# Optimization experiments

Hardware: AMD Instinct MI355X
Metric: run time of the kernel (lower is better)

Reference implementation:

```python
import jax, jax.numpy as jnp
from jax import lax
import numpy as np

B, C, H, W = 8, 256, 64, 64
DSTATE, DCONV, EXPAND = 16, 4, 2
DI = EXPAND * C          # 512 d_inner
DTR = (C + 15) // 16     # 16 dt_rank = ceil(d_model/16)

# ---------- helpers ----------

def _ln(x, g, b):
    m = x.mean(-1, keepdims=True)
    v = x.var(-1, keepdims=True)
    return (x - m) * lax.rsqrt(v + 1e-5) * g + b


def _bn(x, g, b):  # BatchNorm2d, training-mode batch stats
    m = x.mean((0, 2, 3), keepdims=True)
    v = x.var((0, 2, 3), keepdims=True)
    return (x - m) * lax.rsqrt(v + 1e-5) * g[None, :, None, None] + b[None, :, None, None]


def _gn(x, g, b, groups=32):
    Bb, Cc, Hh, Ww = x.shape
    xr = x.reshape(Bb, groups, Cc // groups, Hh, Ww)
    m = xr.mean((2, 3, 4), keepdims=True)
    v = xr.var((2, 3, 4), keepdims=True)
    xr = (xr - m) * lax.rsqrt(v + 1e-5)
    return xr.reshape(Bb, Cc, Hh, Ww) * g[None, :, None, None] + b[None, :, None, None]


def _hsig(x):  # h_sigmoid: relu6(x+3)/6
    return jnp.clip(x + 3.0, 0.0, 6.0) / 6.0


def _axial(v, idx, pos):
    # v: [B,C,N]; pos: [1,C,16] linearly resized to N (align_corners=False == half-pixel)
    N = v.shape[-1]
    pe = jax.image.resize(pos, (1, pos.shape[1], N), method='linear')
    return v + pe + idx  # idx interpolation is identity (same size)


def _dwconvT(x, w):
    # ConvTranspose2d(k=3, stride=2, pad=1, out_pad=1, groups=C) == lhs-dilated corr with flipped kernel
    wf = w[:, :, ::-1, ::-1]
    return lax.conv_general_dilated(x, wf, window_strides=(1, 1), padding=((1, 2), (1, 2)),
                                    lhs_dilation=(2, 2), dimension_numbers=('NCHW', 'OIHW', 'NCHW'),
                                    feature_group_count=x.shape[1])


def _mamba(h, in_w, conv_w, conv_b, xproj_w, dt_w, dt_b, Alog, Dp, out_w):
    # standard mamba_ssm Mamba block forward; h: [B,L,d_model]
    Bb, L, _ = h.shape
    di = in_w.shape[0] // 2
    N = Alog.shape[1]
    dtr = dt_w.shape[1]
    xz = h @ in_w.T                      # [B,L,2*di]
    xm, zg = xz[..., :di], xz[..., di:]
    # causal depthwise conv1d (pad K-1 left == torch pad both + slice [:L])
    xc = lax.conv_general_dilated(xm.transpose(0, 2, 1), conv_w, (1,), [(conv_w.shape[2] - 1, 0)],
                                  dimension_numbers=('NCH', 'OIH', 'NCH'), feature_group_count=di)
    u = jax.nn.silu(xc + conv_b[None, :, None]).transpose(0, 2, 1)  # [B,L,di]
    dbl = u @ xproj_w.T                  # [B,L,dtr+2N]
    dt = jax.nn.softplus(dbl[..., :dtr] @ dt_w.T + dt_b)            # [B,L,di]
    Bm = dbl[..., dtr:dtr + N]
    Cm = dbl[..., dtr + N:]
    A = -jnp.exp(Alog)                   # [di,N]
    dA = jnp.exp(dt[..., None] * A)      # [B,L,di,N]
    dBu = (dt * u)[..., None] * Bm[:, :, None, :]

    def step(hst, inp):
        dA_t, dBu_t = inp
        hst = dA_t * hst + dBu_t
        return hst, hst

    h0 = jnp.zeros((Bb, di, N), dt.dtype)
    _, hs = lax.scan(step, h0, (dA.transpose(1, 0, 2, 3), dBu.transpose(1, 0, 2, 3)))
    y = jnp.einsum('lbdn,bln->bld', hs, Cm) + Dp * u
    y = y * jax.nn.silu(zg)
    return y @ out_w.T


def _forward(x, pos_embed, ln_w, ln_b, proj_w, proj_b,
             up_dw_w, up_bn1_g, up_bn1_b, up_pw_w, up_bn2_g, up_bn2_b,
             down_pw_w, down_bn_g, down_bn_b, gn_g, gn_b,
             f_in_w, f_conv_w, f_conv_b, f_xproj_w, f_dt_w, f_dt_b, f_Alog, f_D, f_out_w,
             b_in_w, b_conv_w, b_conv_b, b_xproj_w, b_dt_w, b_dt_b, b_Alog, b_D, b_out_w):
    # upsample branch: dwconvT -> BN -> ReLU -> 1x1 -> BN -> ReLU6
    z = _dwconvT(x, up_dw_w)
    z = jax.nn.relu(_bn(z, up_bn1_g, up_bn1_b))
    z = jnp.einsum('oc,bchw->bohw', up_pw_w, z)
    z = jnp.clip(_bn(z, up_bn2_g, up_bn2_b), 0.0, 6.0)  # act1 = ReLU6
    dt = x.dtype
    col_max = _ln(_axial(x.max(2), jnp.argmax(x, 2).astype(dt), pos_embed).transpose(0, 2, 1), ln_w, ln_b)
    col_min = _ln(_axial(x.min(2), jnp.argmin(x, 2).astype(dt), pos_embed).transpose(0, 2, 1), ln_w, ln_b)
    row_max = _ln(_axial(x.max(3), jnp.argmax(x, 3).astype(dt), pos_embed).transpose(0, 2, 1), ln_w, ln_b)
    row_min = _ln(_axial(x.min(3), jnp.argmin(x, 3).astype(dt), pos_embed).transpose(0, 2, 1), ln_w, ln_b)
    result_max = jnp.concatenate([col_max, row_max], 1)  # [B, W+H, C]
    result_min = jnp.concatenate([col_min, row_min], 1)
    fpar = (f_in_w, f_conv_w, f_conv_b, f_xproj_w, f_dt_w, f_dt_b, f_Alog, f_D, f_out_w)
    bpar = (b_in_w, b_conv_w, b_conv_b, b_xproj_w, b_dt_w, b_dt_b, b_Alog, b_D, b_out_w)
    fmax = _ln(_mamba(result_max, *fpar), ln_w, ln_b)
    fmin = _ln(_mamba(result_min, *fpar), ln_w, ln_b)
    bmax = _ln(_mamba(jnp.flip(result_max, 1), *bpar), ln_w, ln_b)
    bmin = _ln(_mamba(jnp.flip(result_min, 1), *bpar), ln_w, ln_b)
    res_max = jnp.concatenate([fmax, jnp.flip(bmax, 1)], -1) @ proj_w.T + proj_b
    res_max = _ln(res_max, ln_w, ln_b)
    res_min = jnp.concatenate([fmin, jnp.flip(bmin, 1)], -1) @ proj_w.T + proj_b
    res_min = _ln(res_min, ln_w, ln_b)
    res = res_max[:, :, None, :] + res_min[:, None, :, :]  # [B,L,L,C], L=H+W
    res = res.transpose(0, 3, 1, 2)                        # [B,C,L,L] == [B,C,2H,2W]
    res = _hsig(res) * z
    res = _gn(res, gn_g, gn_b)
    res = jnp.einsum('oc,bchw->bohw', down_pw_w, res[:, :, ::2, ::2])  # 1x1 stride-2 conv
    res = _bn(res, down_bn_g, down_bn_b)
    res = _gn(res, gn_g, gn_b)
    res = res + x
    res = _gn(res, gn_g, gn_b)
    return res


def setup_inputs() -> dict:
    key = jax.random.key(0)
    ks = jax.random.split(key, 32)

    def n(i, shape, s=0.02):
        return jax.random.normal(ks[i], shape, jnp.float32) * s

    inp = {}
    inp['x'] = jax.random.normal(ks[0], (B, C, H, W), jnp.float32)
    inp['pos_embed'] = jax.random.normal(ks[1], (1, C, 16), jnp.float32)
    inp['ln_w'] = jnp.ones((C,), jnp.float32)
    inp['ln_b'] = jnp.zeros((C,), jnp.float32)
    inp['proj_w'] = n(2, (C, 2 * C))
    inp['proj_b'] = jnp.zeros((C,), jnp.float32)
    inp['up_dw_w'] = n(3, (C, 1, 3, 3), 0.1)
    inp['up_bn1_g'] = jnp.ones((C,), jnp.float32)
    inp['up_bn1_b'] = jnp.zeros((C,), jnp.float32)
    inp['up_pw_w'] = n(4, (C, C), 0.05)
    inp['up_bn2_g'] = jnp.ones((C,), jnp.float32)
    inp['up_bn2_b'] = jnp.zeros((C,), jnp.float32)
    inp['down_pw_w'] = n(5, (C, C), 0.05)
    inp['down_bn_g'] = jnp.ones((C,), jnp.float32)
    inp['down_bn_b'] = jnp.zeros((C,), jnp.float32)
    inp['gn_g'] = jnp.ones((C,), jnp.float32)
    inp['gn_b'] = jnp.zeros((C,), jnp.float32)
    Alog = jnp.tile(jnp.log(jnp.arange(1, DSTATE + 1, dtype=jnp.float32))[None, :], (DI, 1))
    dtb = jnp.full((DI,), float(np.log(np.expm1(0.01))), jnp.float32)
    for p, k0 in (('f', 6), ('b', 16)):
        inp[p + '_in_w'] = n(k0, (2 * DI, C))
        inp[p + '_conv_w'] = n(k0 + 1, (DI, 1, DCONV), 0.2)
        inp[p + '_conv_b'] = jnp.zeros((DI,), jnp.float32)
        inp[p + '_xproj_w'] = n(k0 + 2, (DTR + 2 * DSTATE, DI))
        inp[p + '_dt_w'] = n(k0 + 3, (DI, DTR), 0.1)
        inp[p + '_dt_b'] = dtb
        inp[p + '_Alog'] = Alog
        inp[p + '_D'] = jnp.ones((DI,), jnp.float32)
        inp[p + '_out_w'] = n(k0 + 4, (C, DI))
    return inp


def reference(x, pos_embed, ln_w, ln_b, proj_w, proj_b,
              up_dw_w, up_bn1_g, up_bn1_b, up_pw_w, up_bn2_g, up_bn2_b,
              down_pw_w, down_bn_g, down_bn_b, gn_g, gn_b,
              f_in_w, f_conv_w, f_conv_b, f_xproj_w, f_dt_w, f_dt_b, f_Alog, f_D, f_out_w,
              b_in_w, b_conv_w, b_conv_b, b_xproj_w, b_dt_w, b_dt_b, b_Alog, b_D, b_out_w):
    return _forward(x, pos_embed, ln_w, ln_b, proj_w, proj_b,
                    up_dw_w, up_bn1_g, up_bn1_b, up_pw_w, up_bn2_g, up_bn2_b,
                    down_pw_w, down_bn_g, down_bn_b, gn_g, gn_b,
                    f_in_w, f_conv_w, f_conv_b, f_xproj_w, f_dt_w, f_dt_b, f_Alog, f_D, f_out_w,
                    b_in_w, b_conv_w, b_conv_b, b_xproj_w, b_dt_w, b_dt_b, b_Alog, b_D, b_out_w)
```

## Files before the change

kernel.cpp:

```cpp
#include <hip/hip_runtime.h>
#include <hip/hip_bf16.h>

typedef __hip_bfloat16 bf16;
typedef __attribute__((ext_vector_type(8))) short bf16x8v;
typedef __attribute__((ext_vector_type(4))) short bf16x4v;
typedef __attribute__((ext_vector_type(4))) float f32x4v;

#define B_ 8
#define C_ 256
#define L_ 128
#define MB 1048576UL

__device__ inline float b2f(bf16 v){ return __bfloat162float(v); }
__device__ inline bf16 f2b(float v){ return __float2bfloat16(v); }
__device__ inline float siluf(float x){ return x / (1.f + expf(-x)); }
__device__ inline float softplusf(float x){ return (x > 20.f) ? x : log1pf(expf(x)); }
__device__ inline float vclamp(float v){ return fmaxf(v, 0.f) + 1e-5f; }

__device__ inline void bred2(float& a, float& b, float* red){
  int t = threadIdx.x;
  __syncthreads();
  red[t] = a; red[256 + t] = b;
  __syncthreads();
  for (int off = 128; off > 0; off >>= 1){
    if (t < off){ red[t] += red[t + off]; red[256 + t] += red[256 + t + off]; }
    __syncthreads();
  }
  a = red[0]; b = red[256];
}

__device__ inline int tswz(int p, int c){
  return (p*512 + c*2) ^ (((p ^ (p >> 2)) & 7) << 4);
}

__global__ __launch_bounds__(64) void pool1_kernel(const float* __restrict__ x, const float* __restrict__ pos,
    float* __restrict__ pcolmax, float* __restrict__ pcolmin,
    float* __restrict__ prowmax, float* __restrict__ prowmin, float* __restrict__ sxb)
{
  int c = blockIdx.x, b = blockIdx.y, t = threadIdx.x;
  __shared__ float xs[64][65];
  const float* xp = x + ((long)(b*C_ + c))*4096;
  for (int i = 0; i < 64; i++) xs[i][t] = xp[i*64 + t];
  __syncthreads();
  float tt = 0.25f*(float)t - 0.375f;
  const float* pp = pos + c*16;
  float pe;
  if (tt <= 0.f) pe = pp[0];
  else if (tt >= 15.f) pe = pp[15];
  else { int f = (int)floorf(tt); float w = tt - (float)f; pe = pp[f]*(1.f - w) + pp[f+1]*w; }
  float vmax = -1e30f, vmin = 1e30f; int amax = 0, amin = 0;
  for (int j = 0; j < 64; j++){
    float v = xs[t][j];
    if (v > vmax){ vmax = v; amax = j; }
    if (v < vmin){ vmin = v; amin = j; }
  }
  long o = (long)(b*64 + t)*C_ + c;
  prowmax[o] = vmax + pe + (float)amax;
  prowmin[o] = vmin + pe + (float)amin;
  vmax = -1e30f; vmin = 1e30f; amax = 0; amin = 0;
  float sx = 0.f, sx2 = 0.f;
  for (int i = 0; i < 64; i++){
    float v = xs[i][t];
    if (v > vmax){ vmax = v; amax = i; }
    if (v < vmin){ vmin = v; amin = i; }
    sx += v; sx2 += v*v;
  }
  pcolmax[o] = vmax + pe + (float)amax;
  pcolmin[o] = vmin + pe + (float)amin;
  #pragma unroll
  for (int m = 1; m < 64; m <<= 1){ sx += __shfl_xor(sx, m); sx2 += __shfl_xor(sx2, m); }
  if (t == 0){ sxb[(b << 8) + c] = sx; sxb[2048 + (b << 8) + c] = sx2; }
}

__global__ __launch_bounds__(256) void pool2_kernel(const float* __restrict__ pcolmax, const float* __restrict__ pcolmin,
    const float* __restrict__ prowmax, const float* __restrict__ prowmin,
    const float* __restrict__ lnw, const float* __restrict__ lnb, bf16* __restrict__ hbuf)
{
  int r = blockIdx.x, b = blockIdx.y, c = threadIdx.x;
  __shared__ float red[512];
  int p = r & 63;
  long src = (long)(b*64 + p)*C_ + c;
  float vmax = (r < 64) ? pcolmax[src] : prowmax[src];
  float vmin = (r < 64) ? pcolmin[src] : prowmin[src];
  float gw = lnw[c], gb = lnb[c];
  long row = (long)b*L_ + r, frow = (long)b*L_ + (127 - r);
  float s = vmax, s2 = vmax*vmax;
  bred2(s, s2, red);
  float m = s*(1.f/256.f), var = s2*(1.f/256.f) - m*m;
  float o = (vmax - m)*rsqrtf(vclamp(var))*gw + gb;
  hbuf[0*262144 + row*C_ + c]  = f2b(o);
  hbuf[2*262144 + frow*C_ + c] = f2b(o);
  s = vmin; s2 = vmin*vmin;
  bred2(s, s2, red);
  m = s*(1.f/256.f); var = s2*(1.f/256.f) - m*m;
  o = (vmin - m)*rsqrtf(vclamp(var))*gw + gb;
  hbuf[1*262144 + row*C_ + c]  = f2b(o);
  hbuf[3*262144 + frow*C_ + c] = f2b(o);
}

__global__ __launch_bounds__(256) void dwz1_kernel(const float* __restrict__ x, const float* __restrict__ dw,
    bf16* __restrict__ z1, float* __restrict__ bn1sum, float* __restrict__ bn1sq)
{
  int bc = blockIdx.x; int c = bc & 255;
  int tid = threadIdx.x;
  __shared__ float xs[4096];
  const float* xp = x + (long)bc*4096;
  for (int it = 0; it < 16; it++) xs[it*256 + tid] = xp[it*256 + tid];
  float w[9];
  #pragma unroll
  for (int q = 0; q < 9; q++) w[q] = dw[c*9 + q];
  __syncthreads();
  bf16* zp = z1 + (long)bc*16384;
  float s = 0.f, s2 = 0.f;
  for (int it = 0; it < 64; it++){
    int p = it*256 + tid; int i = p >> 7, j = p & 127;
    int xi = i >> 1, xj = j >> 1;
    int io = i & 1, jo = j & 1;
    int xi1 = (xi < 63) ? xi + 1 : 63;
    int xj1 = (xj < 63) ? xj + 1 : 63;
    float XA = xs[xi*64 + xj];
    float XB = xs[xi*64 + xj1];
    float XC = xs[xi1*64 + xj];
    float XD = xs[xi1*64 + xj1];
    float wA = jo ? (io ? w[8] : w[5]) : (io ? w[7] : w[4]);
    float wB = (jo && j < 127) ? (io ? w[6] : w[3]) : 0.f;
    float wC = (io && i < 127) ? (jo ? w[2] : w[1]) : 0.f;
    float wD = (io && jo && i < 127 && j < 127) ? w[0] : 0.f;
    float acc = wA*XA;
    acc += wB*XB;
    acc += wC*XC;
    acc += wD*XD;
    zp[p] = f2b(acc);
    s += acc; s2 += acc*acc;
  }
  __shared__ float red[512];
  bred2(s, s2, red);
  if (tid == 0){ atomicAdd(&bn1sum[c], s); atomicAdd(&bn1sq[c], s2); }
}

__global__ __launch_bounds__(256) void wcvt_all_kernel(
    const float* __restrict__ s0, const float* __restrict__ s1, const float* __restrict__ s2,
    const float* __restrict__ s3, const float* __restrict__ s4, const float* __restrict__ s5,
    const float* __restrict__ s6, const float* __restrict__ s7, const float* __restrict__ s8,
    bf16* __restrict__ d0, bf16* __restrict__ d1, bf16* __restrict__ d2,
    bf16* __restrict__ d3, bf16* __restrict__ d4, bf16* __restrict__ d5,
    bf16* __restrict__ d6, bf16* __restrict__ d7, bf16* __restrict__ d8)
{
  int seg = blockIdx.y;
  const float* s; bf16* d; int n;
  switch (seg){
    case 0: s = s0; d = d0; n = 262144; break;
    case 1: s = s1; d = d1; n = 262144; break;
    case 2: s = s2; d = d2; n = 24576;  break;
    case 3: s = s3; d = d3; n = 24576;  break;
    case 4: s = s4; d = d4; n = 131072; break;
    case 5: s = s5; d = d5; n = 131072; break;
    case 6: s = s6; d = d6; n = 131072; break;
    case 7: s = s7; d = d7; n = 65536;  break;
    default: s = s8; d = d8; n = 65536; break;
  }
  long i = ((long)blockIdx.x*256 + threadIdx.x)*4;
  if (i >= n) return;
  float4 v = *(const float4*)&s[i];
  bf16 o[4] = {f2b(v.x), f2b(v.y), f2b(v.z), f2b(v.w)};
  *(uint2*)&d[i] = *(const uint2*)o;
}

__device__ inline void pwz_gemm_tile(const short* __restrict__ Tbh, const bf16* __restrict__ Wb,
    bf16* __restrict__ z2, float* __restrict__ bn2part,
    int b, int pbase, int slot, int tid)
{
  int wave = tid >> 6, lane = tid & 63;
  int quad = lane >> 4, l16 = lane & 15;
  f32x4v acc[4][4];
  #pragma unroll
  for (int i = 0; i < 4; i++)
    #pragma unroll
    for (int j = 0; j < 4; j++) acc[i][j] = (f32x4v){0.f, 0.f, 0.f, 0.f};
  for (int k0 = 0; k0 < 256; k0 += 32){
    int c = k0 + quad*8;
    bf16x8v a[4], bb[4];
    #pragma unroll
    for (int ms = 0; ms < 4; ms++)
      a[ms] = *(const bf16x8v*)&Wb[(wave*64 + ms*16 + l16)*C_ + c];
    #pragma unroll
    for (int ns = 0; ns < 4; ns++){
      int p = ns*16 + l16;
      bb[ns] = *(const bf16x8v*)((const char*)Tbh + tswz(p, c));
    }
    #pragma unroll
    for (int ms = 0; ms < 4; ms++)
      #pragma unroll
      for (int ns = 0; ns < 4; ns++)
        acc[ms][ns] = __builtin_amdgcn_mfma_f32_16x16x32_bf16(a[ms], bb[ns], acc[ms][ns], 0, 0, 0);
  }
  #pragma unroll
  for (int ms = 0; ms < 4; ms++){
    int o = wave*64 + ms*16 + quad*4;
    #pragma unroll
    for (int r = 0; r < 4; r++){
      long rowbase = ((long)(b*C_ + o + r))*16384 + pbase;
      float s = 0.f, s2 = 0.f;
      #pragma unroll
      for (int ns = 0; ns < 4; ns++){
        bf16 bv = f2b(acc[ms][ns][r]);
        z2[rowbase + ns*16 + l16] = bv;
        float vv = b2f(bv);
        s += vv; s2 += vv*vv;
      }
      #pragma unroll
      for (int m = 1; m < 16; m <<= 1){ s += __shfl_xor(s, m); s2 += __shfl_xor(s2, m); }
      if (l16 == 0){
        atomicAdd(&bn2part[slot*256 + o + r], s);
        atomicAdd(&bn2part[16384 + slot*256 + o + r], s2);
      }
    }
  }
}

__global__ __launch_bounds__(256) void pwz_fused_kernel(const bf16* __restrict__ z1,
    const float* __restrict__ bn1sum, const float* __restrict__ bn1sq,
    const float* __restrict__ g1, const float* __restrict__ b1,
    const bf16* __restrict__ Wb, bf16* __restrict__ z2,
    float* __restrict__ bn2part)
{
  int b = blockIdx.y;
  int p0 = blockIdx.x*128;
  int tid = threadIdx.x;
  __shared__ __align__(16) short Tb[2][16384];
  __shared__ float aa[256], dd[256];
  {
    float m = bn1sum[tid]*(1.f/131072.f);
    float v = bn1sq[tid]*(1.f/131072.f) - m*m;
    float a = g1[tid]*rsqrtf(vclamp(v));
    aa[tid] = a; dd[tid] = b1[tid] - m*a;
  }
  __syncthreads();
  int pc = tid & 15, ch = tid >> 4;
  #pragma unroll
  for (int it = 0; it < 8; it++){
    int c = (ch + it*16)*2;
    const bf16* r0 = &z1[((long)(b*C_ + c))*16384 + p0 + pc*4];
    bf16x4v va = *(const bf16x4v*)r0;
    bf16x4v vb = *(const bf16x4v*)(r0 + 16384);
    float a0 = aa[c], d0 = dd[c], a1 = aa[c+1], d1 = dd[c+1];
    #pragma unroll
    for (int k = 0; k < 4; k++){
      int p = pc*4 + k;
      bf16 h0; *(short*)&h0 = va[k];
      bf16 h1; *(short*)&h1 = vb[k];
      bf16 o0 = f2b(fmaxf(b2f(h0)*a0 + d0, 0.f));
      bf16 o1 = f2b(fmaxf(b2f(h1)*a1 + d1, 0.f));
      unsigned int u = ((unsigned int)(*(unsigned short*)&o1) << 16) | (unsigned int)(*(unsigned short*)&o0);
      *(unsigned int*)((char*)&Tb[0][0] + tswz(p, c)) = u;
    }
  }
  bf16x4v t1a[8], t1b[8];
  #pragma unroll
  for (int it = 0; it < 8; it++){
    int c = (ch + it*16)*2;
    const bf16* r1 = &z1[((long)(b*C_ + c))*16384 + p0 + 64 + pc*4];
    t1a[it] = *(const bf16x4v*)r1;
    t1b[it] = *(const bf16x4v*)(r1 + 16384);
  }
  __syncthreads();
  int slot = (blockIdx.x & 7) | (b << 3);
  pwz_gemm_tile(&Tb[0][0], Wb, z2, bn2part, b, p0, slot, tid);
  #pragma unroll
  for (int it = 0; it < 8; it++){
    int c = (ch + it*16)*2;
    float a0 = aa[c], d0 = dd[c], a1 = aa[c+1], d1 = dd[c+1];
    #pragma unroll
    for (int k = 0; k < 4; k++){
      int p = pc*4 + k;
      bf16 h0; *(short*)&h0 = t1a[it][k];
      bf16 h1; *(short*)&h1 = t1b[it][k];
      bf16 o0 = f2b(fmaxf(b2f(h0)*a0 + d0, 0.f));
      bf16 o1 = f2b(fmaxf(b2f(h1)*a1 + d1, 0.f));
      unsigned int u = ((unsigned int)(*(unsigned short*)&o1) << 16) | (unsigned int)(*(unsigned short*)&o0);
      *(unsigned int*)((char*)&Tb[1][0] + tswz(p, c)) = u;
    }
  }
  __syncthreads();
  pwz_gemm_tile(&Tb[1][0], Wb, z2, bn2part, b, p0 + 64, slot, tid);
}

__global__ __launch_bounds__(256) void inproj_mfma_kernel(const bf16* __restrict__ hb,
    const bf16* __restrict__ Wif, const bf16* __restrict__ Wib2, bf16* __restrict__ xz)
{
  int v = blockIdx.z;
  int m0 = blockIdx.y*256, n0 = blockIdx.x*64;
  const bf16* A = hb + (long)v*262144;
  const bf16* W = (v >= 2) ? Wib2 : Wif;
  bf16* out = xz + (long)v*1048576;
  int tid = threadIdx.x;
  int wave = tid >> 6, lane = tid & 63;
  int quad = lane >> 4, l16 = lane & 15;
  f32x4v acc[4][4];
  #pragma unroll
  for (int i = 0; i < 4; i++)
    #pragma unroll
    for (int j = 0; j < 4; j++) acc[i][j] = (f32x4v){0.f, 0.f, 0.f, 0.f};
  for (int k0 = 0; k0 < 256; k0 += 32){
    int c = k0 + quad*8;
    bf16x8v a[4], bb[4];
    #pragma unroll
    for (int ms = 0; ms < 4; ms++)
      a[ms] = *(const bf16x8v*)&A[(long)(m0 + wave*64 + ms*16 + l16)*256 + c];
    #pragma unroll
    for (int ns = 0; ns < 4; ns++)
      bb[ns] = *(const bf16x8v*)&W[(long)(n0 + ns*16 + l16)*256 + c];
    #pragma unroll
    for (int ms = 0; ms < 4; ms++)
      #pragma unroll
      for (int ns = 0; ns < 4; ns++)
        acc[ms][ns] = __builtin_amdgcn_mfma_f32_16x16x32_bf16(a[ms], bb[ns], acc[ms][ns], 0, 0, 0);
  }
  #pragma unroll
  for (int ms = 0; ms < 4; ms++){
    int m = m0 + wave*64 + ms*16 + quad*4;
    #pragma unroll
    for (int r = 0; r < 4; r++){
      long rowbase = (long)(m + r)*1024 + n0;
      #pragma unroll
      for (int ns = 0; ns < 4; ns++)
        out[rowbase + ns*16 + l16] = f2b(acc[ms][ns][r]);
    }
  }
}

__global__ __launch_bounds__(256) void xproj_mfma_kernel(const bf16* __restrict__ ub,
    const bf16* __restrict__ Wxf, const bf16* __restrict__ Wxb, float* __restrict__ dblb)
{
  int v = blockIdx.y;
  int m0 = blockIdx.x*256;
  const bf16* A = ub + (long)v*524288;
  const bf16* W = (v >= 2) ? Wxb : Wxf;
  float* out = dblb + (long)v*49152;
  int tid = threadIdx.x;
  int wave = tid >> 6, lane = tid & 63;
  int quad = lane >> 4, l16 = lane & 15;
  f32x4v acc[4][3];
  #pragma unroll
  for (int i = 0; i < 4; i++)
    #pragma unroll
    for (int j = 0; j < 3; j++) acc[i][j] = (f32x4v){0.f, 0.f, 0.f, 0.f};
  for (int k0 = 0; k0 < 512; k0 += 32){
    int c = k0 + quad*8;
    bf16x8v a[4], bb[3];
    #pragma unroll
    for (int ms = 0; ms < 4; ms++)
      a[ms] = *(const bf16x8v*)&A[(long)(m0 + wave*64 + ms*16 + l16)*512 + c];
    #pragma unroll
    for (int ns = 0; ns < 3; ns++)
      bb[ns] = *(const bf16x8v*)&W[(long)(ns*16 + l16)*512 + c];
    #pragma unroll
    for (int ms = 0; ms < 4; ms++)
      #pragma unroll
      for (int ns = 0; ns < 3; ns++)
        acc[ms][ns] = __builtin_amdgcn_mfma_f32_16x16x32_bf16(a[ms], bb[ns], acc[ms][ns], 0, 0, 0);
  }
  #pragma unroll
  for (int ms = 0; ms < 4; ms++){
    int m = m0 + wave*64 + ms*16 + quad*4;
    #pragma unroll
    for (int r = 0; r < 4; r++){
      long rowbase = (long)(m + r)*48;
      #pragma unroll
      for (int ns = 0; ns < 3; ns++)
        out[rowbase + ns*16 + l16] = acc[ms][ns][r];
    }
  }
}

__global__ __launch_bounds__(256) void outproj_mfma_kernel(const bf16* __restrict__ yb,
    const bf16* __restrict__ Wof, const bf16* __restrict__ Wob, float* __restrict__ mo)
{
  int v = blockIdx.z;
  int m0 = blockIdx.y*256, n0 = blockIdx.x*64;
  const bf16* A = yb + (long)v*524288;
  const bf16* W = (v >= 2) ? Wob : Wof;
  float* out = mo + (long)v*262144;
  int tid = threadIdx.x;
  int wave = tid >> 6, lane = tid & 63;
  int quad = lane >> 4, l16 = lane & 15;
  f32x4v acc[4][4];
  #pragma unroll
  for (int i = 0; i < 4; i++)
    #pragma unroll
    for (int j = 0; j < 4; j++) acc[i][j] = (f32x4v){0.f, 0.f, 0.f, 0.f};
  for (int k0 = 0; k0 < 512; k0 += 32){
    int c = k0 + quad*8;
    bf16x8v a[4], bb[4];
    #pragma unroll
    for (int ms = 0; ms < 4; ms++)
      a[ms] = *(const bf16x8v*)&A[(long)(m0 + wave*64 + ms*16 + l16)*512 + c];
    #pragma unroll
    for (int ns = 0; ns < 4; ns++)
      bb[ns] = *(const bf16x8v*)&W[(long)(n0 + ns*16 + l16)*512 + c];
    #pragma unroll
    for (int ms = 0; ms < 4; ms++)
      #pragma unroll
      for (int ns = 0; ns < 4; ns++)
        acc[ms][ns] = __builtin_amdgcn_mfma_f32_16x16x32_bf16(a[ms], bb[ns], acc[ms][ns], 0, 0, 0);
  }
  #pragma unroll
  for (int ms = 0; ms < 4; ms++){
    int m = m0 + wave*64 + ms*16 + quad*4;
    #pragma unroll
    for (int r = 0; r < 4; r++){
      long rowbase = (long)(m + r)*256 + n0;
      #pragma unroll
      for (int ns = 0; ns < 4; ns++)
        out[rowbase + ns*16 + l16] = acc[ms][ns][r];
    }
  }
}

__global__ __launch_bounds__(256) void pj_mfma_kernel(const bf16* __restrict__ cb,
    const bf16* __restrict__ Wp, const float* __restrict__ pb, float* __restrict__ rp)
{
  int z = blockIdx.z;
  int m0 = blockIdx.y*256, n0 = blockIdx.x*64;
  const bf16* A = cb + (long)z*524288;
  float* out = rp + (long)z*262144;
  int tid = threadIdx.x;
  int wave = tid >> 6, lane = tid & 63;
  int quad = lane >> 4, l16 = lane & 15;
  f32x4v acc[4][4];
  #pragma unroll
  for (int i = 0; i < 4; i++)
    #pragma unroll
    for (int j = 0; j < 4; j++) acc[i][j] = (f32x4v){0.f, 0.f, 0.f, 0.f};
  for (int k0 = 0; k0 < 512; k0 += 32){
    int c = k0 + quad*8;
    bf16x8v a[4], bb[4];
    #pragma unroll
    for (int ms = 0; ms < 4; ms++)
      a[ms] = *(const bf16x8v*)&A[(long)(m0 + wave*64 + ms*16 + l16)*512 + c];
    #pragma unroll
    for (int ns = 0; ns < 4; ns++)
      bb[ns] = *(const bf16x8v*)&Wp[(long)(n0 + ns*16 + l16)*512 + c];
    #pragma unroll
    for (int ms = 0; ms < 4; ms++)
      #pragma unroll
      for (int ns = 0; ns < 4; ns++)
        acc[ms][ns] = __builtin_amdgcn_mfma_f32_16x16x32_bf16(a[ms], bb[ns], acc[ms][ns], 0, 0, 0);
  }
  #pragma unroll
  for (int ms = 0; ms < 4; ms++){
    int m = m0 + wave*64 + ms*16 + quad*4;
    #pragma unroll
    for (int r = 0; r < 4; r++){
      long rowbase = (long)(m + r)*256 + n0;
      #pragma unroll
      for (int ns = 0; ns < 4; ns++)
        out[rowbase + ns*16 + l16] = acc[ms][ns][r] + pb[n0 + ns*16 + l16];
    }
  }
}

__global__ __launch_bounds__(256) void gemm_kernel(
  const float* __restrict__ Abase, long sA, int lda,
  const float* __restrict__ W0, const float* __restrict__ W1,
  const float* __restrict__ bias0, const float* __restrict__ bias1, int wsplit,
  float* __restrict__ Cbase, long sC, int ldc,
  int M, int N, int K, int act)
{
  int z = blockIdx.z;
  const float* A = Abase + (long)z*sA;
  float* Cp = Cbase + (long)z*sC;
  const float* W = (z >= wsplit) ? W1 : W0;
  const float* bias = (z >= wsplit) ? bias1 : bias0;
  int m0 = blockIdx.y*64, n0 = blockIdx.x*64;
  __shared__ __align__(16) float As[16][68];
  __shared__ __align__(16) float Ws[16][68];
  int tid = threadIdx.x, tx = tid & 15, ty = tid >> 4;
  float acc[4][4] = {};
  for (int k0 = 0; k0 < K; k0 += 16){
    #pragma unroll
    for (int q = 0; q < 4; q++){
      int e = tid + q*256; int r = e >> 4, kk = e & 15;
      int mi = m0 + r, ki = k0 + kk;
      As[kk][r] = (mi < M && ki < K) ? A[(long)mi*lda + ki] : 0.f;
    }
    #pragma unroll
    for (int q = 0; q < 4; q++){
      int e = tid + q*256; int n = e >> 4, kk = e & 15;
      int ni = n0 + n, ki = k0 + kk;
      Ws[kk][n] = (ni < N && ki < K) ? W[(long)ni*K + ki] : 0.f;
    }
    __syncthreads();
    #pragma unroll
    for (int kk = 0; kk < 16; kk++){
      float4 a4 = *(const float4*)&As[kk][ty*4];
      float4 b4 = *(const float4*)&Ws[kk][tx*4];
      float av[4] = {a4.x, a4.y, a4.z, a4.w};
      float bv[4] = {b4.x, b4.y, b4.z, b4.w};
      #pragma unroll
      for (int mm = 0; mm < 4; mm++)
        #pragma unroll
        for (int nn = 0; nn < 4; nn++) acc[mm][nn] += av[mm]*bv[nn];
    }
    __syncthreads();
  }
  #pragma unroll
  for (int mm = 0; mm < 4; mm++){
    int mi = m0 + ty*4 + mm;
    if (mi >= M) continue;
    #pragma unroll
    for (int nn = 0; nn < 4; nn++){
      int ni = n0 + tx*4 + nn;
      if (ni >= N) continue;
      float v = acc[mm][nn];
      if (bias) v += bias[ni];
      if (act == 2) v = softplusf(v);
      Cp[(long)mi*ldc + ni] = v;
    }
  }
}

__global__ __launch_bounds__(512) void conv1d_kernel(const bf16* __restrict__ xzb,
    const float* __restrict__ fw, const float* __restrict__ fb,
    const float* __restrict__ bw, const float* __restrict__ bb,
    bf16* __restrict__ ub)
{
  int l = blockIdx.x, b = blockIdx.y, v = blockIdx.z, d = threadIdx.x;
  const bf16* xm = xzb + (long)v*1024*1024;
  const float* w  = (v < 2) ? fw : bw;
  const float* cb = (v < 2) ? fb : bb;
  float acc = cb[d];
  #pragma unroll
  for (int k = 0; k < 4; k++){
    int ll = l - 3 + k;
    if (ll >= 0) acc += b2f(xm[(long)(b*L_ + ll)*1024 + d]) * w[d*4 + k];
  }
  ub[(long)v*1024*512 + (long)(b*L_ + l)*512 + d] = f2b(siluf(acc));
}

__global__ __launch_bounds__(64) void scan_kernel(const float* __restrict__ dtb, const bf16* __restrict__ ub,
    const float* __restrict__ dblb, const bf16* __restrict__ xzb,
    const float* __restrict__ fAlog, const float* __restrict__ fD,
    const float* __restrict__ bAlog, const float* __restrict__ bD,
    bf16* __restrict__ yb)
{
  int v = blockIdx.z, b = blockIdx.y;
  int tid = threadIdx.x;
  int dd = tid & 15, qtr = tid >> 4;
  int d0 = blockIdx.x*16;
  int d = d0 + dd;
  const float* dt  = dtb  + (long)v*1024*512;
  const bf16*  u   = ub   + (long)v*1024*512;
  const float* dbl = dblb + (long)v*1024*48;
  const bf16*  zg  = xzb  + (long)v*1024*1024 + 512;
  const float* Alog = (v < 2) ? fAlog : bAlog;
  const float* Dp   = (v < 2) ? fD : bD;
  __shared__ bf16 sdt[2048], su[2048], szg[2048];
  __shared__ __align__(16) bf16 sbc[4096];
  long row = (long)b*L_;
  for (int idx = tid; idx < 2048; idx += 64){
    int l = idx >> 4, j = idx & 15;
    sdt[idx] = f2b(dt[(row + l)*512 + d0 + j]);
    su [idx] = u[(row + l)*512 + d0 + j];
    szg[idx] = zg[(row + l)*1024 + d0 + j];
  }
  for (int idx = tid; idx < 4096; idx += 64){
    int l = idx >> 5, j = idx & 31;
    sbc[idx] = f2b(dbl[(row + l)*48 + 16 + j]);
  }
  float a2[4];
  #pragma unroll
  for (int n = 0; n < 4; n++) a2[n] = -expf(Alog[d*16 + qtr*4 + n]) * 1.44269504f;
  float Dv = Dp[d];
  float h[4];
  #pragma unroll
  for (int n = 0; n < 4; n++) h[n] = 0.f;
  __syncthreads();
  bf16* yo = yb + (long)v*1024*512;
  for (int l = 0; l < 128; l++){
    float dtv = b2f(sdt[l*16 + dd]);
    float uv  = b2f(su [l*16 + dd]);
    float zgv = b2f(szg[l*16 + dd]);
    bf16x4v Bv = *(const bf16x4v*)&sbc[l*32 + qtr*4];
    bf16x4v Cv = *(const bf16x4v*)&sbc[l*32 + 16 + qtr*4];
    float dtu = dtv*uv;
    float acc = 0.f;
    #pragma unroll
    for (int n = 0; n < 4; n++){
      float dA = exp2f(dtv*a2[n]);
      bf16 tb; *(short*)&tb = Bv[n];
      bf16 tc; *(short*)&tc = Cv[n];
      h[n] = dA*h[n] + dtu*b2f(tb);
      acc += h[n]*b2f(tc);
    }
    acc += __shfl_xor(acc, 16);
    acc += __shfl_xor(acc, 32);
    if (qtr == 0)
      yo[(row + l)*512 + d] = f2b((acc + Dv*uv) * siluf(zgv));
  }
}

__global__ __launch_bounds__(256) void ln_kernel(const float* __restrict__ inb, bf16* __restrict__ outb0,
    bf16* __restrict__ outb1, float* __restrict__ outf,
    const float* __restrict__ lnw, const float* __restrict__ lnb, int mode)
{
  int r = blockIdx.x, b = blockIdx.y, v = blockIdx.z, c = threadIdx.x;
  long row = (long)b*L_ + r;
  float val = inb[((long)v*1024 + row)*C_ + c];
  __shared__ float red[512];
  float s = val, s2 = val*val;
  bred2(s, s2, red);
  float m = s*(1.f/256.f), var = s2*(1.f/256.f) - m*m;
  float o = (val - m)*rsqrtf(vclamp(var))*lnw[c] + lnb[c];
  if (mode == 1){
    long frow = (long)b*L_ + (127 - r);
    if (v == 0)      outb0[row*512 + c] = f2b(o);
    else if (v == 1) outb1[row*512 + c] = f2b(o);
    else if (v == 2) outb0[frow*512 + 256 + c] = f2b(o);
    else             outb1[frow*512 + 256 + c] = f2b(o);
  } else {
    outf[((long)v*1024 + row)*C_ + c] = o;
  }
}

__global__ __launch_bounds__(256) void hsig_kernel(bf16* __restrict__ z2, const float* __restrict__ rm,
    const float* __restrict__ rn, const float* __restrict__ bn2part,
    const float* __restrict__ g2, const float* __restrict__ b2,
    float* __restrict__ gnsum, float* __restrict__ gnsq)
{
  int c = blockIdx.x, b = blockIdx.y, tid = threadIdx.x;
  __shared__ float red[512];
  float pa = 0.f, pb = 0.f;
  if (tid < 64){ pa = bn2part[tid*256 + c]; pb = bn2part[16384 + tid*256 + c]; }
  bred2(pa, pb, red);
  float mm2 = pa*(1.f/131072.f);
  float vv2 = pb*(1.f/131072.f) - mm2*mm2;
  float aa = g2[c] * rsqrtf(vclamp(vv2));
  float dd = b2[c] - mm2*aa;
  __shared__ float rms[128], rns[128];
  if (tid < 128){
    rms[tid] = rm[(long)(b*L_ + tid)*C_ + c];
    rns[tid] = rn[(long)(b*L_ + tid)*C_ + c];
  }
  __syncthreads();
  bf16* zp = z2 + ((long)(b*C_ + c))*16384;
  float s = 0.f, s2 = 0.f;
  for (int g = 0; g < 16; g++){
    float tv[4]; int wq[4];
    #pragma unroll
    for (int q = 0; q < 4; q++){
      int p = g*1024 + q*256 + tid; int i = p >> 7, j = p & 127;
      float zv = b2f(zp[p])*aa + dd;
      zv = fminf(fmaxf(zv, 0.f), 6.f);
      float gate = rms[i] + rns[j];
      gate = fminf(fmaxf(gate + 3.f, 0.f), 6.f) * (1.f/6.f);
      float t = gate*zv;
      s += t; s2 += t*t;
      tv[q] = t;
      wq[q] = (((i | j) & 1) == 0) ? ((i >> 1)*64 + (j >> 1)) : -1;
    }
    __syncthreads();
    #pragma unroll
    for (int q = 0; q < 4; q++)
      if (wq[q] >= 0) zp[wq[q]] = f2b(tv[q]);
  }
  bred2(s, s2, red);
  if (tid == 0){ atomicAdd(&gnsum[b*32 + (c >> 3)], s); atomicAdd(&gnsq[b*32 + (c >> 3)], s2); }
}

__global__ __launch_bounds__(256) void pwdown_fused_kernel(const bf16* __restrict__ z2,
    const float* __restrict__ gnsum, const float* __restrict__ gnsq,
    const float* __restrict__ gn_g, const float* __restrict__ gn_b,
    const bf16* __restrict__ Wb, const float* __restrict__ x,
    float* __restrict__ out, float* __restrict__ sds)
{
  int b = blockIdx.y;
  int p0 = blockIdx.x*64;
  int tid = threadIdx.x;
  __shared__ __align__(16) short Tb[16384];
  __shared__ float gA[256], gD[256];
  {
    float m = gnsum[b*32 + (tid >> 3)]*(1.f/131072.f);
    float v = gnsq[b*32 + (tid >> 3)]*(1.f/131072.f) - m*m;
    float A = rsqrtf(vclamp(v))*gn_g[tid];
    gA[tid] = A; gD[tid] = gn_b[tid] - m*A;
  }
  __syncthreads();
  {
    int pc = tid & 15, ch = tid >> 4;
    #pragma unroll
    for (int it = 0; it < 8; it++){
      int c2 = ch + it*16;
      int c = c2*2;
      const bf16* r0 = &z2[((long)(b*C_ + c))*16384 + p0 + pc*4];
      bf16x4v va = *(const bf16x4v*)r0;
      bf16x4v vb = *(const bf16x4v*)(r0 + 16384);
      float a0 = gA[c], d0 = gD[c];
      float a1 = gA[c + 1], d1 = gD[c + 1];
      #pragma unroll
      for (int k = 0; k < 4; k++){
        int p = pc*4 + k;
        bf16 h0; *(short*)&h0 = va[k];
        bf16 h1; *(short*)&h1 = vb[k];
        bf16 o0 = f2b(b2f(h0)*a0 + d0);
        bf16 o1 = f2b(b2f(h1)*a1 + d1);
        unsigned int u = ((unsigned int)(*(unsigned short*)&o1) << 16) | (unsigned int)(*(unsigned short*)&o0);
        *(unsigned int*)((char*)Tb + tswz(p, c)) = u;
      }
    }
  }
  __syncthreads();
  int wave = tid >> 6, lane = tid & 63;
  int quad = lane >> 4, l16 = lane & 15;
  f32x4v acc[4][4];
  #pragma unroll
  for (int i = 0; i < 4; i++)
    #pragma unroll
    for (int j = 0; j < 4; j++) acc[i][j] = (f32x4v){0.f, 0.f, 0.f, 0.f};
  for (int k0 = 0; k0 < 256; k0 += 32){
    int c = k0 + quad*8;
    bf16x8v a[4], bb[4];
    #pragma unroll
    for (int ms = 0; ms < 4; ms++)
      a[ms] = *(const bf16x8v*)&Wb[(wave*64 + ms*16 + l16)*C_ + c];
    #pragma unroll
    for (int ns = 0; ns < 4; ns++){
      int p = ns*16 + l16;
      bb[ns] = *(const bf16x8v*)((const char*)Tb + tswz(p, c));
    }
    #pragma unroll
    for (int ms = 0; ms < 4; ms++)
      #pragma unroll
      for (int ns = 0; ns < 4; ns++)
        acc[ms][ns] = __builtin_amdgcn_mfma_f32_16x16x32_bf16(a[ms], bb[ns], acc[ms][ns], 0, 0, 0);
  }
  #pragma unroll
  for (int ms = 0; ms < 4; ms++){
    int o = wave*64 + ms*16 + quad*4;
    #pragma unroll
    for (int r = 0; r < 4; r++){
      long rowbase = ((long)(b*C_ + o + r))*4096 + p0;
      float sd = 0.f, sd2 = 0.f, sdx = 0.f;
      #pragma unroll
      for (int ns = 0; ns < 4; ns++){
        float v = acc[ms][ns][r];
        out[rowbase + ns*16 + l16] = v;
        float xv = x[rowbase + ns*16 + l16];
        sd += v; sd2 += v*v; sdx += v*xv;
      }
      #pragma unroll
      for (int m = 1; m < 16; m <<= 1){
        sd += __shfl_xor(sd, m); sd2 += __shfl_xor(sd2, m); sdx += __shfl_xor(sdx, m);
      }
      if (l16 == 0){
        int oc = (b << 8) + o + r;
        atomicAdd(&sds[oc], sd);
        atomicAdd(&sds[2048 + oc], sd2);
        atomicAdd(&sds[4096 + oc], sdx);
      }
    }
  }
}

__global__ __launch_bounds__(256) void final_kernel(const float* __restrict__ x,
    const float* __restrict__ sds, const float* __restrict__ sxb,
    const float* __restrict__ dbn_g, const float* __restrict__ dbn_b,
    const float* __restrict__ gn_g, const float* __restrict__ gn_b,
    float* __restrict__ out)
{
  int c = blockIdx.x, b = blockIdx.y, tid = threadIdx.x;
  __shared__ float lv[11][8];
  int g8 = (c >> 3) << 3;
  if (tid < 8){
    int cc = g8 + tid;
    float sd = 0.f, sd2 = 0.f;
    for (int bb2 = 0; bb2 < 8; bb2++){ sd += sds[bb2*256 + cc]; sd2 += sds[2048 + bb2*256 + cc]; }
    float mB = sd*(1.f/32768.f);
    float vB = sd2*(1.f/32768.f) - mB*mB;
    float ab = dbn_g[cc] * rsqrtf(vclamp(vB));
    float db = dbn_b[cc] - mB*ab;
    float inv_n = 1.f/4096.f;
    float m = sds[b*256 + cc]*inv_n, Ed2 = sds[2048 + b*256 + cc]*inv_n;
    float mx = sxb[b*256 + cc]*inv_n, Ex2 = sxb[2048 + b*256 + cc]*inv_n;
    float Edx = sds[4096 + b*256 + cc]*inv_n;
    float Ev = ab*m + db;
    float Ev2 = ab*ab*Ed2 + 2.f*ab*db*m + db*db;
    lv[0][tid] = ab; lv[1][tid] = db; lv[2][tid] = m; lv[3][tid] = Ed2;
    lv[4][tid] = mx; lv[5][tid] = Ex2; lv[6][tid] = Edx; lv[7][tid] = Ev; lv[8][tid] = Ev2;
  }
  __syncthreads();
  if (tid < 8){
    float m1 = 0.f, q1 = 0.f;
    for (int k = 0; k < 8; k++){ m1 += lv[7][k]; q1 += lv[8][k]; }
    m1 *= 0.125f; q1 *= 0.125f;
    int cc = g8 + tid;
    float inv1 = rsqrtf(vclamp(q1 - m1*m1));
    float A1 = inv1*gn_g[cc];
    float D1 = gn_b[cc] - m1*A1;
    float ab = lv[0][tid], db = lv[1][tid];
    float m = lv[2][tid], Ed2 = lv[3][tid], mx = lv[4][tid], Ex2 = lv[5][tid], Edx = lv[6][tid];
    float al = A1*ab;
    float be = A1*db + D1;
    float Et = al*m + be + mx;
    float Et2 = al*al*Ed2 + 2.f*al*be*m + be*be + 2.f*al*Edx + 2.f*be*mx + Ex2;
    lv[9][tid] = Et; lv[10][tid] = Et2; lv[0][tid] = al; lv[1][tid] = be;
  }
  __syncthreads();
  float m2 = 0.f, q2 = 0.f;
  for (int k = 0; k < 8; k++){ m2 += lv[9][k]; q2 += lv[10][k]; }
  m2 *= 0.125f; q2 *= 0.125f;
  float G = rsqrtf(vclamp(q2 - m2*m2))*gn_g[c];
  float P = G*lv[0][c & 7];
  float Q = G;
  float R = G*(lv[1][c & 7] - m2) + gn_b[c];
  long base = ((long)(b*C_ + c))*4096;
  for (int it = 0; it < 16; it++){
    long idx = base + it*256 + tid;
    out[idx] = P*out[idx] + Q*x[idx] + R;
  }
}

extern "C" void kernel_launch(void* const* d_in, const int* in_sizes, int n_in,
                              void* d_out, int out_size, void* d_ws, size_t ws_size,
                              hipStream_t stream)
{
  (void)in_sizes; (void)n_in; (void)out_size; (void)ws_size;
  const float* x         = (const float*)d_in[0];
  const float* pos       = (const float*)d_in[1];
  const float* ln_w      = (const float*)d_in[2];
  const float* ln_b      = (const float*)d_in[3];
  const float* proj_w    = (const float*)d_in[4];
  const float* proj_b    = (const float*)d_in[5];
  const float* up_dw_w   = (const float*)d_in[6];
  const float* up_bn1_g  = (const float*)d_in[7];
  const float* up_bn1_b  = (const float*)d_in[8];
  const float* up_pw_w   = (const float*)d_in[9];
  const float* up_bn2_g  = (const float*)d_in[10];
  const float* up_bn2_b  = (const float*)d_in[11];
  const float* down_pw_w = (const float*)d_in[12];
  const float* down_bn_g = (const float*)d_in[13];
  const float* down_bn_b = (const float*)d_in[14];
  const float* gn_g      = (const float*)d_in[15];
  const float* gn_b      = (const float*)d_in[16];
  const float* f_in_w    = (const float*)d_in[17];
  const float* f_conv_w  = (const float*)d_in[18];
  const float* f_conv_b  = (const float*)d_in[19];
  const float* f_xproj_w = (const float*)d_in[20];
  const float* f_dt_w    = (const float*)d_in[21];
  const float* f_dt_b    = (const float*)d_in[22];
  const float* f_Alog    = (const float*)d_in[23];
  const float* f_D       = (const float*)d_in[24];
  const float* f_out_w   = (const float*)d_in[25];
  const float* b_in_w    = (const float*)d_in[26];
  const float* b_conv_w  = (const float*)d_in[27];
  const float* b_conv_b  = (const float*)d_in[28];
  const float* b_xproj_w = (const float*)d_in[29];
  const float* b_dt_w    = (const float*)d_in[30];
  const float* b_dt_b    = (const float*)d_in[31];
  const float* b_Alog    = (const float*)d_in[32];
  const float* b_D       = (const float*)d_in[33];
  const float* b_out_w   = (const float*)d_in[34];

  char* sb = (char*)d_ws;
  float* statz  = (float*)(sb);
  float* sds    = (float*)(sb + 6144);
  float* bn2part= (float*)(sb + 32768);
  float* sxb    = (float*)(sb + 184320);
  float* rmrn  = (float*)(sb + 1*MB);
  bf16*  Wbbuf = (bf16*)(sb + 3*MB);
  bf16*  Wb2buf= (bf16*)(sb + 3*MB + 262144);
  bf16*  Wpb   = (bf16*)(sb + 3*MB + 524288);
  char* big = sb + 4*MB;
  float* pool4  = (float*)(big + 0*MB);
  bf16*  hbufb  = (bf16*)(big + 2*MB);
  bf16*  Wif    = (bf16*)(big + 4*MB);
  bf16*  Wib2   = (bf16*)(big + 4*MB + 524288);
  bf16*  Wxf    = (bf16*)(big + 5*MB);
  bf16*  Wxb    = (bf16*)(big + 5*MB + 65536);
  bf16*  Wof    = (bf16*)(big + 5*MB + 131072);
  bf16*  Wob    = (bf16*)(big + 5*MB + 393216);
  bf16*  xzbuf  = (bf16*)(big + 6*MB);
  bf16*  ubuf   = (bf16*)(big + 22*MB);
  float* dblbuf = (float*)(big + 30*MB);
  float* dtbuf  = (float*)(big + 31*MB);
  bf16*  ybuf   = (bf16*)(big + 39*MB);
  float* mout   = (float*)(big + 47*MB);
  bf16*  cbufb  = (bf16*)(big + 51*MB);
  float* respre = (float*)(big + 55*MB);
  bf16*  z1buf  = (bf16*)(big);
  bf16*  z2buf  = (bf16*)(big);
  float* dbuf   = (float*)d_out;

  float* bn1sum = statz;        float* bn1sq = statz + 256;
  float* gnsum  = statz + 1024; float* gnsq  = statz + 1280;
  float* pcolmax = pool4;
  float* pcolmin = pool4 + 131072;
  float* prowmax = pool4 + 262144;
  float* prowmin = pool4 + 393216;

  hipMemsetAsync(statz, 0, 163840, stream);

  wcvt_all_kernel<<<dim3(256, 9), 256, 0, stream>>>(
      f_in_w, b_in_w, f_xproj_w, b_xproj_w, f_out_w, b_out_w, proj_w, up_pw_w, down_pw_w,
      Wif, Wib2, Wxf, Wxb, Wof, Wob, Wpb, Wbbuf, Wb2buf);

  pool1_kernel<<<dim3(256, 8), 64, 0, stream>>>(x, pos, pcolmax, pcolmin, prowmax, prowmin, sxb);
  pool2_kernel<<<dim3(128, 8), 256, 0, stream>>>(pcolmax, pcolmin, prowmax, prowmin, ln_w, ln_b, hbufb);
  inproj_mfma_kernel<<<dim3(16, 4, 4), 256, 0, stream>>>(hbufb, Wif, Wib2, xzbuf);
  conv1d_kernel<<<dim3(128, 8, 4), 512, 0, stream>>>(xzbuf, f_conv_w, f_conv_b, b_conv_w, b_conv_b, ubuf);
  xproj_mfma_kernel<<<dim3(4, 4), 256, 0, stream>>>(ubuf, Wxf, Wxb, dblbuf);
  gemm_kernel<<<dim3(8, 16, 4), 256, 0, stream>>>(dblbuf, 49152, 48, f_dt_w, b_dt_w, f_dt_b, b_dt_b, 2,
                                                  dtbuf, 524288, 512, 1024, 512, 16, 2);
  scan_kernel<<<dim3(32, 8, 4), 64, 0, stream>>>(dtbuf, ubuf, dblbuf, xzbuf, f_Alog, f_D, b_Alog, b_D, ybuf);
  outproj_mfma_kernel<<<dim3(4, 4, 4), 256, 0, stream>>>(ybuf, Wof, Wob, mout);
  ln_kernel<<<dim3(128, 8, 4), 256, 0, stream>>>(mout, cbufb, cbufb + 524288, nullptr, ln_w, ln_b, 1);
  pj_mfma_kernel<<<dim3(4, 4, 2), 256, 0, stream>>>(cbufb, Wpb, proj_b, respre);
  ln_kernel<<<dim3(128, 8, 2), 256, 0, stream>>>(respre, nullptr, nullptr, rmrn, ln_w, ln_b, 0);

  dwz1_kernel<<<2048, 256, 0, stream>>>(x, up_dw_w, z1buf, bn1sum, bn1sq);
  pwz_fused_kernel<<<dim3(128, 8), 256, 0, stream>>>(z1buf, bn1sum, bn1sq, up_bn1_g, up_bn1_b,
                                                     Wbbuf, z2buf, bn2part);

  hsig_kernel<<<dim3(256, 8), 256, 0, stream>>>(z2buf, rmrn, rmrn + 262144, bn2part,
                                                up_bn2_g, up_bn2_b, gnsum, gnsq);
  pwdown_fused_kernel<<<dim3(64, 8), 256, 0, stream>>>(z2buf, gnsum, gnsq, gn_g, gn_b,
                                                       Wb2buf, x, dbuf, sds);
  final_kernel<<<dim3(256, 8), 256, 0, stream>>>(x, sds, sxb, down_bn_g, down_bn_b, gn_g, gn_b,
                                                 (float*)d_out);
}
```

Before: 512.0 us.

## Use wave-shuffle block reductions, split pwz tiles, drop hsig in-loop barriers

The block reduction helper now does a 64-lane shuffle tree per wave and a single shared-memory combine of four partials, replacing the log-step shared-memory tree that had a barrier per step. The fused pointwise GEMM kernel now processes one 64-pixel tile per block over twice as many blocks, instead of two tiles with a manually prefetched second tile. The hsig kernel loads the first 4096 pixels, the only ones its in-place downsampled writes overwrite, into registers before a single barrier, which removes the per-iteration barrier. The trade-offs are a reduction helper that is hard-wired to 256-thread blocks and the loss of load/compute overlap in the pwz kernel.

```diff
diff --git a/kernel.cpp b/kernel.cpp
--- a/kernel.cpp
+++ b/kernel.cpp
@@ -18,15 +18,14 @@
 __device__ inline float vclamp(float v){ return fmaxf(v, 0.f) + 1e-5f; }
 
 __device__ inline void bred2(float& a, float& b, float* red){
-  int t = threadIdx.x;
-  __syncthreads();
-  red[t] = a; red[256 + t] = b;
-  __syncthreads();
-  for (int off = 128; off > 0; off >>= 1){
-    if (t < off){ red[t] += red[t + off]; red[256 + t] += red[256 + t + off]; }
-    __syncthreads();
-  }
-  a = red[0]; b = red[256];
+  #pragma unroll
+  for (int m = 1; m < 64; m <<= 1){ a += __shfl_xor(a, m); b += __shfl_xor(b, m); }
+  int tid = threadIdx.x, wave = tid >> 6, lane = tid & 63;
+  __syncthreads();
+  if (lane == 0){ red[wave] = a; red[8 + wave] = b; }
+  __syncthreads();
+  a = red[0] + red[1] + red[2] + red[3];
+  b = red[8] + red[9] + red[10] + red[11];
 }
 
 __device__ inline int tswz(int p, int c){
@@ -77,7 +76,7 @@
     const float* __restrict__ lnw, const float* __restrict__ lnb, bf16* __restrict__ hbuf)
 {
   int r = blockIdx.x, b = blockIdx.y, c = threadIdx.x;
-  __shared__ float red[512];
+  __shared__ float red[16];
   int p = r & 63;
   long src = (long)(b*64 + p)*C_ + c;
   float vmax = (r < 64) ? pcolmax[src] : prowmax[src];
@@ -133,7 +132,7 @@
     zp[p] = f2b(acc);
     s += acc; s2 += acc*acc;
   }
-  __shared__ float red[512];
+  __shared__ float red[16];
   bred2(s, s2, red);
   if (tid == 0){ atomicAdd(&bn1sum[c], s); atomicAdd(&bn1sq[c], s2); }
 }
@@ -166,10 +165,46 @@
   *(uint2*)&d[i] = *(const uint2*)o;
 }
 
-__device__ inline void pwz_gemm_tile(const short* __restrict__ Tbh, const bf16* __restrict__ Wb,
-    bf16* __restrict__ z2, float* __restrict__ bn2part,
-    int b, int pbase, int slot, int tid)
-{
+__global__ __launch_bounds__(256) void pwz_fused_kernel(const bf16* __restrict__ z1,
+    const float* __restrict__ bn1sum, const float* __restrict__ bn1sq,
+    const float* __restrict__ g1, const float* __restrict__ b1,
+    const bf16* __restrict__ Wb, bf16* __restrict__ z2,
+    float* __restrict__ bn2part)
+{
+  int b = blockIdx.y;
+  int p0 = blockIdx.x*64;
+  int tid = threadIdx.x;
+  __shared__ __align__(16) short Tb[16384];
+  __shared__ float aa[256], dd[256];
+  {
+    float m = bn1sum[tid]*(1.f/131072.f);
+    float v = bn1sq[tid]*(1.f/131072.f) - m*m;
+    float a = g1[tid]*rsqrtf(vclamp(v));
+    aa[tid] = a; dd[tid] = b1[tid] - m*a;
+  }
+  __syncthreads();
+  {
+    int pc = tid & 15, ch = tid >> 4;
+    #pragma unroll
+    for (int it = 0; it < 8; it++){
+      int c = (ch + it*16)*2;
+      const bf16* r0 = &z1[((long)(b*C_ + c))*16384 + p0 + pc*4];
+      bf16x4v va = *(const bf16x4v*)r0;
+      bf16x4v vb = *(const bf16x4v*)(r0 + 16384);
+      float a0 = aa[c], d0 = dd[c], a1 = aa[c+1], d1 = dd[c+1];
+      #pragma unroll
+      for (int k = 0; k < 4; k++){
+        int p = pc*4 + k;
+        bf16 h0; *(short*)&h0 = va[k];
+        bf16 h1; *(short*)&h1 = vb[k];
+        bf16 o0 = f2b(fmaxf(b2f(h0)*a0 + d0, 0.f));
+        bf16 o1 = f2b(fmaxf(b2f(h1)*a1 + d1, 0.f));
+        unsigned int u = ((unsigned int)(*(unsigned short*)&o1) << 16) | (unsigned int)(*(unsigned short*)&o0);
+        *(unsigned int*)((char*)Tb + tswz(p, c)) = u;
+      }
+    }
+  }
+  __syncthreads();
   int wave = tid >> 6, lane = tid & 63;
   int quad = lane >> 4, l16 = lane & 15;
   f32x4v acc[4][4];
@@ -186,7 +221,7 @@
     #pragma unroll
     for (int ns = 0; ns < 4; ns++){
       int p = ns*16 + l16;
-      bb[ns] = *(const bf16x8v*)((const char*)Tbh + tswz(p, c));
+      bb[ns] = *(const bf16x8v*)((const char*)Tb + tswz(p, c));
     }
     #pragma unroll
     for (int ms = 0; ms < 4; ms++)
@@ -194,12 +229,13 @@
       for (int ns = 0; ns < 4; ns++)
         acc[ms][ns] = __builtin_amdgcn_mfma_f32_16x16x32_bf16(a[ms], bb[ns], acc[ms][ns], 0, 0, 0);
   }
+  int slot = (blockIdx.x & 7) | (b << 3);
   #pragma unroll
   for (int ms = 0; ms < 4; ms++){
     int o = wave*64 + ms*16 + quad*4;
     #pragma unroll
     for (int r = 0; r < 4; r++){
-      long rowbase = ((long)(b*C_ + o + r))*16384 + pbase;
+      long rowbase = ((long)(b*C_ + o + r))*16384 + p0;
       float s = 0.f, s2 = 0.f;
       #pragma unroll
       for (int ns = 0; ns < 4; ns++){
@@ -216,73 +252,6 @@
       }
     }
   }
-}
-
-__global__ __launch_bounds__(256) void pwz_fused_kernel(const bf16* __restrict__ z1,
-    const float* __restrict__ bn1sum, const float* __restrict__ bn1sq,
-    const float* __restrict__ g1, const float* __restrict__ b1,
-    const bf16* __restrict__ Wb, bf16* __restrict__ z2,
-    float* __restrict__ bn2part)
-{
-  int b = blockIdx.y;
-  int p0 = blockIdx.x*128;
-  int tid = threadIdx.x;
-  __shared__ __align__(16) short Tb[2][16384];
-  __shared__ float aa[256], dd[256];
-  {
-    float m = bn1sum[tid]*(1.f/131072.f);
-    float v = bn1sq[tid]*(1.f/131072.f) - m*m;
-    float a = g1[tid]*rsqrtf(vclamp(v));
-    aa[tid] = a; dd[tid] = b1[tid] - m*a;
-  }
-  __syncthreads();
-  int pc = tid & 15, ch = tid >> 4;
-  #pragma unroll
-  for (int it = 0; it < 8; it++){
-    int c = (ch + it*16)*2;
-    const bf16* r0 = &z1[((long)(b*C_ + c))*16384 + p0 + pc*4];
-    bf16x4v va = *(const bf16x4v*)r0;
-    bf16x4v vb = *(const bf16x4v*)(r0 + 16384);
-    float a0 = aa[c], d0 = dd[c], a1 = aa[c+1], d1 = dd[c+1];
-    #pragma unroll
-    for (int k = 0; k < 4; k++){
-      int p = pc*4 + k;
-      bf16 h0; *(short*)&h0 = va[k];
-      bf16 h1; *(short*)&h1 = vb[k];
-      bf16 o0 = f2b(fmaxf(b2f(h0)*a0 + d0, 0.f));
-      bf16 o1 = f2b(fmaxf(b2f(h1)*a1 + d1, 0.f));
-      unsigned int u = ((unsigned int)(*(unsigned short*)&o1) << 16) | (unsigned int)(*(unsigned short*)&o0);
-      *(unsigned int*)((char*)&Tb[0][0] + tswz(p, c)) = u;
-    }
-  }
-  bf16x4v t1a[8], t1b[8];
-  #pragma unroll
-  for (int it = 0; it < 8; it++){
-    int c = (ch + it*16)*2;
-    const bf16* r1 = &z1[((long)(b*C_ + c))*16384 + p0 + 64 + pc*4];
-    t1a[it] = *(const bf16x4v*)r1;
-    t1b[it] = *(const bf16x4v*)(r1 + 16384);
-  }
-  __syncthreads();
-  int slot = (blockIdx.x & 7) | (b << 3);
-  pwz_gemm_tile(&Tb[0][0], Wb, z2, bn2part, b, p0, slot, tid);
-  #pragma unroll
-  for (int it = 0; it < 8; it++){
-    int c = (ch + it*16)*2;
-    float a0 = aa[c], d0 = dd[c], a1 = aa[c+1], d1 = dd[c+1];
-    #pragma unroll
-    for (int k = 0; k < 4; k++){
-      int p = pc*4 + k;
-      bf16 h0; *(short*)&h0 = t1a[it][k];
-      bf16 h1; *(short*)&h1 = t1b[it][k];
-      bf16 o0 = f2b(fmaxf(b2f(h0)*a0 + d0, 0.f));
-      bf16 o1 = f2b(fmaxf(b2f(h1)*a1 + d1, 0.f));
-      unsigned int u = ((unsigned int)(*(unsigned short*)&o1) << 16) | (unsigned int)(*(unsigned short*)&o0);
-      *(unsigned int*)((char*)&Tb[1][0] + tswz(p, c)) = u;
-    }
-  }
-  __syncthreads();
-  pwz_gemm_tile(&Tb[1][0], Wb, z2, bn2part, b, p0 + 64, slot, tid);
 }
 
 __global__ __launch_bounds__(256) void inproj_mfma_kernel(const bf16* __restrict__ hb,
@@ -607,7 +576,7 @@
   int r = blockIdx.x, b = blockIdx.y, v = blockIdx.z, c = threadIdx.x;
   long row = (long)b*L_ + r;
   float val = inb[((long)v*1024 + row)*C_ + c];
-  __shared__ float red[512];
+  __shared__ float red[16];
   float s = val, s2 = val*val;
   bred2(s, s2, red);
   float m = s*(1.f/256.f), var = s2*(1.f/256.f) - m*m;
@@ -629,7 +598,12 @@
     float* __restrict__ gnsum, float* __restrict__ gnsq)
 {
   int c = blockIdx.x, b = blockIdx.y, tid = threadIdx.x;
-  __shared__ float red[512];
+  __shared__ float red[16];
+  __shared__ float rms[128], rns[128];
+  if (tid < 128){
+    rms[tid] = rm[(long)(b*L_ + tid)*C_ + c];
+    rns[tid] = rn[(long)(b*L_ + tid)*C_ + c];
+  }
   float pa = 0.f, pb = 0.f;
   if (tid < 64){ pa = bn2part[tid*256 + c]; pb = bn2part[16384 + tid*256 + c]; }
   bred2(pa, pb, red);
@@ -637,16 +611,30 @@
   float vv2 = pb*(1.f/131072.f) - mm2*mm2;
   float aa = g2[c] * rsqrtf(vclamp(vv2));
   float dd = b2[c] - mm2*aa;
-  __shared__ float rms[128], rns[128];
-  if (tid < 128){
-    rms[tid] = rm[(long)(b*L_ + tid)*C_ + c];
-    rns[tid] = rn[(long)(b*L_ + tid)*C_ + c];
-  }
-  __syncthreads();
   bf16* zp = z2 + ((long)(b*C_ + c))*16384;
+  float pre[16];
+  #pragma unroll
+  for (int g = 0; g < 4; g++)
+    #pragma unroll
+    for (int q = 0; q < 4; q++)
+      pre[g*4 + q] = b2f(zp[g*1024 + q*256 + tid]);
+  __syncthreads();
   float s = 0.f, s2 = 0.f;
-  for (int g = 0; g < 16; g++){
-    float tv[4]; int wq[4];
+  #pragma unroll
+  for (int g = 0; g < 4; g++){
+    #pragma unroll
+    for (int q = 0; q < 4; q++){
+      int p = g*1024 + q*256 + tid; int i = p >> 7, j = p & 127;
+      float zv = pre[g*4 + q]*aa + dd;
+      zv = fminf(fmaxf(zv, 0.f), 6.f);
+      float gate = rms[i] + rns[j];
+      gate = fminf(fmaxf(gate + 3.f, 0.f), 6.f) * (1.f/6.f);
+      float t = gate*zv;
+      s += t; s2 += t*t;
+      if (((i | j) & 1) == 0) zp[(i >> 1)*64 + (j >> 1)] = f2b(t);
+    }
+  }
+  for (int g = 4; g < 16; g++){
     #pragma unroll
     for (int q = 0; q < 4; q++){
       int p = g*1024 + q*256 + tid; int i = p >> 7, j = p & 127;
@@ -656,13 +644,8 @@
       gate = fminf(fmaxf(gate + 3.f, 0.f), 6.f) * (1.f/6.f);
       float t = gate*zv;
       s += t; s2 += t*t;
-      tv[q] = t;
-      wq[q] = (((i | j) & 1) == 0) ? ((i >> 1)*64 + (j >> 1)) : -1;
-    }
-    __syncthreads();
-    #pragma unroll
-    for (int q = 0; q < 4; q++)
-      if (wq[q] >= 0) zp[wq[q]] = f2b(tv[q]);
+      if (((i | j) & 1) == 0) zp[(i >> 1)*64 + (j >> 1)] = f2b(t);
+    }
   }
   bred2(s, s2, red);
   if (tid == 0){ atomicAdd(&gnsum[b*32 + (c >> 3)], s); atomicAdd(&gnsq[b*32 + (c >> 3)], s2); }
@@ -918,7 +901,7 @@
   ln_kernel<<<dim3(128, 8, 2), 256, 0, stream>>>(respre, nullptr, nullptr, rmrn, ln_w, ln_b, 0);
 
   dwz1_kernel<<<2048, 256, 0, stream>>>(x, up_dw_w, z1buf, bn1sum, bn1sq);
-  pwz_fused_kernel<<<dim3(128, 8), 256, 0, stream>>>(z1buf, bn1sum, bn1sq, up_bn1_g, up_bn1_b,
+  pwz_fused_kernel<<<dim3(256, 8), 256, 0, stream>>>(z1buf, bn1sum, bn1sq, up_bn1_g, up_bn1_b,
                                                      Wbbuf, z2buf, bn2part);
 
   hsig_kernel<<<dim3(256, 8), 256, 0, stream>>>(z2buf, rmrn, rmrn + 262144, bn2part,
```

New measurement: 508.2 us. About the same (-0.7%).
